# Performance work log

Hardware: AMD Instinct MI355X
Metric: run time of the kernel (lower is better)

## Reference

```python
import jax, jax.numpy as jnp
import numpy as np

EMBED_DIM = 1024
NUM_HEADS = 16
D_K = EMBED_DIM // NUM_HEADS
SEQ = 4096
BATCH = 1


def setup_inputs() -> dict:
    key = jax.random.key(0)
    ks = jax.random.split(key, 9)
    s = 1.0 / np.sqrt(EMBED_DIM)
    return {
        "x": jax.random.normal(ks[0], (BATCH, SEQ, EMBED_DIM), dtype=jnp.float32),
        "Wq": jax.random.normal(ks[1], (EMBED_DIM, EMBED_DIM), dtype=jnp.float32) * s,
        "bq": jax.random.normal(ks[2], (EMBED_DIM,), dtype=jnp.float32) * 0.02,
        "Wk": jax.random.normal(ks[3], (EMBED_DIM, EMBED_DIM), dtype=jnp.float32) * s,
        "bk": jax.random.normal(ks[4], (EMBED_DIM,), dtype=jnp.float32) * 0.02,
        "Wv": jax.random.normal(ks[5], (EMBED_DIM, EMBED_DIM), dtype=jnp.float32) * s,
        "bv": jax.random.normal(ks[6], (EMBED_DIM,), dtype=jnp.float32) * 0.02,
        "Wo": jax.random.normal(ks[7], (EMBED_DIM, EMBED_DIM), dtype=jnp.float32) * s,
        "bo": jax.random.normal(ks[8], (EMBED_DIM,), dtype=jnp.float32) * 0.02,
    }


def reference(x, Wq, bq, Wk, bk, Wv, bv, Wo, bo):
    B, S, E = x.shape
    H, Dk = NUM_HEADS, D_K

    def split_heads(t):  # [B,S,E] -> [B,H,S,Dk]
        return t.reshape(B, S, H, Dk).transpose(0, 2, 1, 3)

    Q = split_heads(x @ Wq.T + bq)
    K = split_heads(x @ Wk.T + bk)
    V = split_heads(x @ Wv.T + bv)

    scores = jnp.einsum("bhqd,bhkd->bhqk", Q, K) / jnp.sqrt(jnp.float32(Dk))
    causal = jnp.tril(jnp.ones((S, S), dtype=bool))
    scores = jnp.where(causal, scores, -jnp.inf)
    attn = jax.nn.softmax(scores, axis=-1)
    out = jnp.einsum("bhqk,bhkd->bhqd", attn, V)  # [B,H,S,Dk]
    out = out.transpose(0, 2, 1, 3).reshape(B, S, E)
    return out @ Wo.T + bo
```

## Files before the change

### kernel.cpp

```cpp
#include <hip/hip_runtime.h>
#include <hip/hip_bf16.h>
#include <math.h>

#define SEQ 4096
#define EMB 1024
#define NH  16
#define DK  64

typedef __attribute__((ext_vector_type(8))) unsigned short us8;
typedef __attribute__((ext_vector_type(8))) short         s8;
typedef __attribute__((ext_vector_type(4))) unsigned short us4;
typedef __attribute__((ext_vector_type(4))) float          f4;

static __device__ __forceinline__ unsigned short f2bf(float f) {
    union { float f; unsigned u; } v; v.f = f;
    unsigned r = v.u + 0x7FFF + ((v.u >> 16) & 1);
    return (unsigned short)(r >> 16);
}

__device__ __forceinline__ void gl2lds16(const void* g, void* l) {
    __builtin_amdgcn_global_load_lds((const __attribute__((address_space(1))) void*)g,
                                     (__attribute__((address_space(3))) void*)l, 16, 0, 0);
}

__device__ __forceinline__ int pkbf(float a, float b) {
    return (int)__builtin_amdgcn_perm(__float_as_uint(a), __float_as_uint(b), 0x07060302u);
}

__global__ void cvt_all(const float* __restrict__ x,
                        const float* __restrict__ w0, const float* __restrict__ w1,
                        const float* __restrict__ w2, const float* __restrict__ w3,
                        unsigned short* __restrict__ xo,
                        unsigned short* __restrict__ o0, unsigned short* __restrict__ o1,
                        unsigned short* __restrict__ o2, unsigned short* __restrict__ o3) {
    const int idx = blockIdx.x * 256 + threadIdx.x;
    const float* in;
    unsigned short* out;
    int off;
    if (idx < (1 << 20)) { in = x; out = xo; off = idx; }
    else {
        const int t = idx - (1 << 20);
        const int w = t >> 18;
        off = t & ((1 << 18) - 1);
        in  = w == 0 ? w0 : (w == 1 ? w1 : (w == 2 ? w2 : w3));
        out = w == 0 ? o0 : (w == 1 ? o1 : (w == 2 ? o2 : o3));
    }
    const float4 v = ((const float4*)in)[off];
    us4 o;
    o[0] = f2bf(v.x); o[1] = f2bf(v.y); o[2] = f2bf(v.z); o[3] = f2bf(v.w);
    ((us4*)out)[off] = o;
}

__global__ __launch_bounds__(256) void transpose_kernel(
    const unsigned short* __restrict__ in, unsigned short* __restrict__ out) {
    __shared__ unsigned short t[64][72];
    const int tid = threadIdx.x;
    const int row = tid >> 2, c = (tid & 3) * 16;
    const int gr = blockIdx.x * 64, gc = blockIdx.y * 64;
    const unsigned short* src = in + (size_t)(gr + row) * EMB + gc + c;
    *(us8*)&t[row][c]     = *(const us8*)src;
    *(us8*)&t[row][c + 8] = *(const us8*)(src + 8);
    __syncthreads();
    us8 o0, o1;
#pragma unroll
    for (int j = 0; j < 8; ++j) { o0[j] = t[c + j][row]; o1[j] = t[c + 8 + j][row]; }
    unsigned short* dst = out + (size_t)(gc + row) * SEQ + gr + c;
    *(us8*)dst       = o0;
    *(us8*)(dst + 8) = o1;
}

__global__ __launch_bounds__(256) void qkv_gemm(
    const unsigned short* __restrict__ X,
    const unsigned short* __restrict__ Wq, const unsigned short* __restrict__ Wk,
    const unsigned short* __restrict__ Wv,
    const float* __restrict__ bq, const float* __restrict__ bk, const float* __restrict__ bv,
    unsigned short* __restrict__ Qo, unsigned short* __restrict__ Ko, unsigned short* __restrict__ Vo)
{
    __shared__ unsigned short As[128 * 64];
    __shared__ unsigned short Bs[128 * 64];

    const int region = blockIdx.y >> 3;
    const unsigned short* W   = region == 0 ? Wq : (region == 1 ? Wk : Wv);
    const float*         bias = region == 0 ? bq : (region == 1 ? bk : bv);
    unsigned short*      out  = region == 0 ? Qo : (region == 1 ? Ko : Vo);
    const float scale = region == 0 ? 0.18033688011112042f : 1.0f;

    const int tid  = threadIdx.x;
    const int wave = tid >> 6;
    const int lane = tid & 63;
    const int quad = lane >> 4;
    const int l16  = lane & 15;
    const int wm   = (wave >> 1) * 64;
    const int wn   = (wave & 1) * 64;
    const int bm   = blockIdx.x * 128;
    const int bn   = (blockIdx.y & 7) * 128;

    f4 acc[4][4];
#pragma unroll
    for (int a = 0; a < 4; ++a)
#pragma unroll
        for (int b = 0; b < 4; ++b) acc[a][b] = (f4){0, 0, 0, 0};

    const int rsub = lane >> 3;
    const int gc   = ((lane & 7) ^ rsub) * 8;
    const int swz  = l16 & 7;

    for (int k0 = 0; k0 < EMB; k0 += 64) {
        __syncthreads();
#pragma unroll
        for (int i = 0; i < 4; ++i) {
            const int cb = i * 4 + wave;
            const int r  = cb * 8 + rsub;
            gl2lds16(X + (size_t)(bm + r) * EMB + k0 + gc, &As[cb * 512]);
            gl2lds16(W + (size_t)(bn + r) * EMB + k0 + gc, &Bs[cb * 512]);
        }
        __syncthreads();
#pragma unroll
        for (int kc = 0; kc < 2; ++kc) {
            s8 af[4], bf[4];
#pragma unroll
            for (int t = 0; t < 4; ++t) {
                const int seg = (kc * 4 + quad) ^ swz;
                af[t] = *(const s8*)&As[(wm + t * 16 + l16) * 64 + seg * 8];
                bf[t] = *(const s8*)&Bs[(wn + t * 16 + l16) * 64 + seg * 8];
            }
#pragma unroll
            for (int tm = 0; tm < 4; ++tm)
#pragma unroll
                for (int tn = 0; tn < 4; ++tn)
                    acc[tm][tn] = __builtin_amdgcn_mfma_f32_16x16x32_bf16(af[tm], bf[tn], acc[tm][tn], 0, 0, 0);
        }
    }

#pragma unroll
    for (int tn = 0; tn < 4; ++tn) {
        const int n = bn + wn + tn * 16 + l16;
        const float bv2 = bias[n];
#pragma unroll
        for (int tm = 0; tm < 4; ++tm)
#pragma unroll
            for (int rr = 0; rr < 4; ++rr) {
                const int m = bm + wm + tm * 16 + quad * 4 + rr;
                out[(size_t)m * EMB + n] = f2bf((acc[tm][tn][rr] + bv2) * scale);
            }
    }
}

__global__ __launch_bounds__(256) void gemm_op(
    const unsigned short* __restrict__ A, const unsigned short* __restrict__ B,
    const float* __restrict__ bias, float* __restrict__ C)
{
    __shared__ unsigned short As[128 * 64];
    __shared__ unsigned short Bs[64 * 64];

    const int tid  = threadIdx.x;
    const int wave = tid >> 6;
    const int lane = tid & 63;
    const int quad = lane >> 4;
    const int l16  = lane & 15;
    const int wm   = (wave >> 1) * 64;
    const int wn   = (wave & 1) * 32;
    const int bm   = blockIdx.x * 128;
    const int bn   = blockIdx.y * 64;

    f4 acc[4][2];
#pragma unroll
    for (int a = 0; a < 4; ++a) { acc[a][0] = (f4){0,0,0,0}; acc[a][1] = (f4){0,0,0,0}; }

    const int rsub = lane >> 3;
    const int gc   = ((lane & 7) ^ rsub) * 8;
    const int swz  = l16 & 7;

    for (int k0 = 0; k0 < EMB; k0 += 64) {
        __syncthreads();
#pragma unroll
        for (int i = 0; i < 6; ++i) {
            const int cb = i * 4 + wave;
            if (cb < 16) {
                gl2lds16(A + (size_t)(bm + cb * 8 + rsub) * EMB + k0 + gc, &As[cb * 512]);
            } else {
                const int c2 = cb - 16;
                gl2lds16(B + (size_t)(bn + c2 * 8 + rsub) * EMB + k0 + gc, &Bs[c2 * 512]);
            }
        }
        __syncthreads();
#pragma unroll
        for (int kc = 0; kc < 2; ++kc) {
            const int seg = (kc * 4 + quad) ^ swz;
            s8 af[4], bf[2];
#pragma unroll
            for (int t = 0; t < 4; ++t)
                af[t] = *(const s8*)&As[(wm + t * 16 + l16) * 64 + seg * 8];
#pragma unroll
            for (int t = 0; t < 2; ++t)
                bf[t] = *(const s8*)&Bs[(wn + t * 16 + l16) * 64 + seg * 8];
#pragma unroll
            for (int tm = 0; tm < 4; ++tm)
#pragma unroll
                for (int tn = 0; tn < 2; ++tn)
                    acc[tm][tn] = __builtin_amdgcn_mfma_f32_16x16x32_bf16(af[tm], bf[tn], acc[tm][tn], 0, 0, 0);
        }
    }

#pragma unroll
    for (int tn = 0; tn < 2; ++tn) {
        const int n = bn + wn + tn * 16 + l16;
        const float bv2 = bias[n];
#pragma unroll
        for (int tm = 0; tm < 4; ++tm)
#pragma unroll
            for (int rr = 0; rr < 4; ++rr) {
                const int m = bm + wm + tm * 16 + quad * 4 + rr;
                C[(size_t)m * EMB + n] = acc[tm][tn][rr] + bv2;
            }
    }
}

__global__ __launch_bounds__(256) void attn_kernel(
    const unsigned short* __restrict__ Qg, const unsigned short* __restrict__ Kg,
    const unsigned short* __restrict__ Vtg, unsigned short* __restrict__ Og)
{
    __shared__ unsigned short Ks[2][64][72];
    __shared__ unsigned short Vs[2][64][72];

    const int tid  = threadIdx.x;
    const int wave = tid >> 6;
    const int lane = tid & 63;
    const int quad = lane >> 4;
    const int l16  = lane & 15;
    const int h    = blockIdx.x;
    const int y    = blockIdx.y;
    const int g    = y >> 4, u = y & 15;
    const int tile = g == 0 ? 63 - u : (g == 1 ? 32 + u : (g == 2 ? 31 - u : u));
    const int colbase = h * DK;
    const int wrow0 = tile * 64 + wave * 16;
    const int q_own = wrow0 + l16;

    s8 qf[2];
    {
        const unsigned short* q = Qg + (size_t)q_own * EMB + colbase + quad * 8;
        qf[0] = *(const s8*)(q);
        qf[1] = *(const s8*)(q + 32);
    }

    const int row = tid >> 2;
    const int c0  = (tid & 3) * 16;
    const int a_    = c0 >> 4;
    const int vcol0 = (a_ >> 1) * 32 + (a_ & 1) * 4;

    const unsigned short* kptr = Kg  + (size_t)row * EMB + colbase + c0;
    const unsigned short* vptr = Vtg + (size_t)(colbase + row) * SEQ + c0;

    const int jmax = tile;
    us8 kr0 = *(const us8*)kptr, kr1 = *(const us8*)(kptr + 8);
    us8 vr0 = *(const us8*)vptr, vr1 = *(const us8*)(vptr + 8);
    {
        *(us8*)&Ks[0][row][c0]     = kr0;
        *(us8*)&Ks[0][row][c0 + 8] = kr1;
        us4 w0, w1, w2, w3;
#pragma unroll
        for (int i = 0; i < 4; ++i) { w0[i] = vr0[i]; w1[i] = vr0[4+i]; w2[i] = vr1[i]; w3[i] = vr1[4+i]; }
        *(us4*)&Vs[0][row][vcol0]      = w0;
        *(us4*)&Vs[0][row][vcol0 + 8]  = w1;
        *(us4*)&Vs[0][row][vcol0 + 16] = w2;
        *(us4*)&Vs[0][row][vcol0 + 24] = w3;
    }
    kr0 = *(const us8*)(kptr + (size_t)64 * EMB);
    kr1 = *(const us8*)(kptr + (size_t)64 * EMB + 8);
    vr0 = *(const us8*)(vptr + 64);
    vr1 = *(const us8*)(vptr + 64 + 8);

    float l_i = 0.0f;
    f4 o[4];
#pragma unroll
    for (int t = 0; t < 4; ++t) o[t] = (f4){0, 0, 0, 0};

    for (int j = 0; j <= jmax; ++j) {
        __syncthreads();
        const int cur = j & 1;
        if (j < jmax) {
            const int nxt = cur ^ 1;
            *(us8*)&Ks[nxt][row][c0]     = kr0;
            *(us8*)&Ks[nxt][row][c0 + 8] = kr1;
            us4 w0, w1, w2, w3;
#pragma unroll
            for (int i = 0; i < 4; ++i) { w0[i] = vr0[i]; w1[i] = vr0[4+i]; w2[i] = vr1[i]; w3[i] = vr1[4+i]; }
            *(us4*)&Vs[nxt][row][vcol0]      = w0;
            *(us4*)&Vs[nxt][row][vcol0 + 8]  = w1;
            *(us4*)&Vs[nxt][row][vcol0 + 16] = w2;
            *(us4*)&Vs[nxt][row][vcol0 + 24] = w3;
            if (j + 1 < jmax) {
                const unsigned short* kn = kptr + (size_t)(j + 2) * 64 * EMB;
                const unsigned short* vn = vptr + (j + 2) * 64;
                kr0 = *(const us8*)kn;  kr1 = *(const us8*)(kn + 8);
                vr0 = *(const us8*)vn;  vr1 = *(const us8*)(vn + 8);
            }
        }

        f4 s[4] = { {0,0,0,0}, {0,0,0,0}, {0,0,0,0}, {0,0,0,0} };
#pragma unroll
        for (int kc = 0; kc < 2; ++kc)
#pragma unroll
            for (int t = 0; t < 4; ++t) {
                s8 kv = *(const s8*)&Ks[cur][t * 16 + l16][kc * 32 + quad * 8];
                s[t] = __builtin_amdgcn_mfma_f32_16x16x32_bf16(kv, qf[kc], s[t], 0, 0, 0);
            }

        if (j == jmax) {
#pragma unroll
            for (int t = 0; t < 4; ++t) {
                const int kb = j * 64 + t * 16 + quad * 4;
#pragma unroll
                for (int r = 0; r < 4; ++r)
                    if (kb + r > q_own) s[t][r] = -1e30f;
            }
        }

        float rs = 0.0f;
#pragma unroll
        for (int t = 0; t < 4; ++t)
#pragma unroll
            for (int r = 0; r < 4; ++r) {
                const float p = __builtin_amdgcn_exp2f(s[t][r]);
                s[t][r] = p;
                rs += p;
            }
        rs += __shfl_xor(rs, 16);
        rs += __shfl_xor(rs, 32);
        l_i += rs;

        union { int i[8]; s8 v[2]; } pku;
#pragma unroll
        for (int t = 0; t < 4; ++t) {
            pku.i[t * 2]     = pkbf(s[t][1], s[t][0]);
            pku.i[t * 2 + 1] = pkbf(s[t][3], s[t][2]);
        }

#pragma unroll
        for (int kc = 0; kc < 2; ++kc)
#pragma unroll
            for (int t = 0; t < 4; ++t) {
                s8 va = *(const s8*)&Vs[cur][t * 16 + l16][kc * 32 + quad * 8];
                o[t] = __builtin_amdgcn_mfma_f32_16x16x32_bf16(va, pku.v[kc], o[t], 0, 0, 0);
            }
    }

    const float inv = 1.0f / l_i;
#pragma unroll
    for (int t = 0; t < 4; ++t) {
        us4 ov;
#pragma unroll
        for (int r = 0; r < 4; ++r) ov[r] = f2bf(o[t][r] * inv);
        *(us4*)&Og[(size_t)q_own * EMB + colbase + t * 16 + quad * 4] = ov;
    }
}

extern "C" void kernel_launch(void* const* d_in, const int* in_sizes, int n_in,
                              void* d_out, int out_size, void* d_ws, size_t ws_size,
                              hipStream_t stream) {
    const float* x  = (const float*)d_in[0];
    const float* Wq = (const float*)d_in[1];
    const float* bq = (const float*)d_in[2];
    const float* Wk = (const float*)d_in[3];
    const float* bk = (const float*)d_in[4];
    const float* Wv = (const float*)d_in[5];
    const float* bv = (const float*)d_in[6];
    const float* Wo = (const float*)d_in[7];
    const float* bo = (const float*)d_in[8];
    float* out = (float*)d_out;

    unsigned short* ws = (unsigned short*)d_ws;
    unsigned short* xb  = ws;
    unsigned short* Wqb = xb  + (size_t)SEQ * EMB;
    unsigned short* Wkb = Wqb + (size_t)EMB * EMB;
    unsigned short* Wvb = Wkb + (size_t)EMB * EMB;
    unsigned short* Wob = Wvb + (size_t)EMB * EMB;
    unsigned short* Qb  = Wob + (size_t)EMB * EMB;
    unsigned short* Kb  = Qb  + (size_t)SEQ * EMB;
    unsigned short* Vtb = Kb  + (size_t)SEQ * EMB;
    unsigned short* Ab  = Vtb + (size_t)SEQ * EMB;

    cvt_all<<<8192, 256, 0, stream>>>(x, Wq, Wk, Wv, Wo, xb, Wqb, Wkb, Wvb, Wob);

    qkv_gemm<<<dim3(SEQ / 128, 24), 256, 0, stream>>>(xb, Wqb, Wkb, Wvb, bq, bk, bv, Qb, Kb, Ab);

    transpose_kernel<<<dim3(SEQ / 64, EMB / 64), 256, 0, stream>>>(Ab, Vtb);

    attn_kernel<<<dim3(NH, 64), 256, 0, stream>>>(Qb, Kb, Vtb, Ab);

    gemm_op<<<dim3(SEQ / 128, EMB / 64), 256, 0, stream>>>(Ab, Wob, bo, out);
}
```

Measured before the change: 216.3 us.

## Pair complementary causal query tiles per attention block and move V column permute into transpose

Each attention block now runs 512 threads covering two query tiles (u and 63-u), so every block does an equal amount of causal work and shares the same K/V tile loads between both tiles. Waves for the shorter tile skip compute once their diagonal is reached but still help load shared tiles. The V column permutation used by the MFMA layout moves from the attention kernel's LDS store into the transpose kernel's global store, which simplifies the per-iteration staging to one 16-byte store each for K and V. The trade-off is larger blocks with idle waves in later iterations and fewer blocks in the grid.

```diff
diff --git a/kernel.cpp b/kernel.cpp
--- a/kernel.cpp
+++ b/kernel.cpp
@@ -64,9 +64,16 @@
     us8 o0, o1;
 #pragma unroll
     for (int j = 0; j < 8; ++j) { o0[j] = t[c + j][row]; o1[j] = t[c + 8 + j][row]; }
-    unsigned short* dst = out + (size_t)(gc + row) * SEQ + gr + c;
-    *(us8*)dst       = o0;
-    *(us8*)(dst + 8) = o1;
+    const int a_   = c >> 4;
+    const int base = (a_ >> 1) * 32 + (a_ & 1) * 4;
+    us4 g0, g1, g2, g3;
+#pragma unroll
+    for (int i = 0; i < 4; ++i) { g0[i] = o0[i]; g1[i] = o0[4 + i]; g2[i] = o1[i]; g3[i] = o1[4 + i]; }
+    unsigned short* dst = out + (size_t)(gc + row) * SEQ + gr + base;
+    *(us4*)dst        = g0;
+    *(us4*)(dst + 8)  = g1;
+    *(us4*)(dst + 16) = g2;
+    *(us4*)(dst + 24) = g3;
 }
 
 __global__ __launch_bounds__(256) void qkv_gemm(
@@ -216,7 +223,7 @@
     }
 }
 
-__global__ __launch_bounds__(256) void attn_kernel(
+__global__ __launch_bounds__(512) void attn_kernel(
     const unsigned short* __restrict__ Qg, const unsigned short* __restrict__ Kg,
     const unsigned short* __restrict__ Vtg, unsigned short* __restrict__ Og)
 {
@@ -230,10 +237,12 @@
     const int l16  = lane & 15;
     const int h    = blockIdx.x;
     const int y    = blockIdx.y;
-    const int g    = y >> 4, u = y & 15;
-    const int tile = g == 0 ? 63 - u : (g == 1 ? 32 + u : (g == 2 ? 31 - u : u));
+    const int u    = (y < 16) ? y : 47 - y;
+    const int jmax = 63 - u;
+    const int tileMine = (wave < 4) ? (63 - u) : u;
+    const int jmine    = (wave < 4) ? jmax : u;
     const int colbase = h * DK;
-    const int wrow0 = tile * 64 + wave * 16;
+    const int wrow0 = tileMine * 64 + (wave & 3) * 16;
     const int q_own = wrow0 + l16;
 
     s8 qf[2];
@@ -243,32 +252,17 @@
         qf[1] = *(const s8*)(q + 32);
     }
 
-    const int row = tid >> 2;
-    const int c0  = (tid & 3) * 16;
-    const int a_    = c0 >> 4;
-    const int vcol0 = (a_ >> 1) * 32 + (a_ & 1) * 4;
-
+    const int row = tid >> 3;
+    const int c0  = (tid & 7) * 8;
     const unsigned short* kptr = Kg  + (size_t)row * EMB + colbase + c0;
     const unsigned short* vptr = Vtg + (size_t)(colbase + row) * SEQ + c0;
 
-    const int jmax = tile;
-    us8 kr0 = *(const us8*)kptr, kr1 = *(const us8*)(kptr + 8);
-    us8 vr0 = *(const us8*)vptr, vr1 = *(const us8*)(vptr + 8);
-    {
-        *(us8*)&Ks[0][row][c0]     = kr0;
-        *(us8*)&Ks[0][row][c0 + 8] = kr1;
-        us4 w0, w1, w2, w3;
-#pragma unroll
-        for (int i = 0; i < 4; ++i) { w0[i] = vr0[i]; w1[i] = vr0[4+i]; w2[i] = vr1[i]; w3[i] = vr1[4+i]; }
-        *(us4*)&Vs[0][row][vcol0]      = w0;
-        *(us4*)&Vs[0][row][vcol0 + 8]  = w1;
-        *(us4*)&Vs[0][row][vcol0 + 16] = w2;
-        *(us4*)&Vs[0][row][vcol0 + 24] = w3;
-    }
-    kr0 = *(const us8*)(kptr + (size_t)64 * EMB);
-    kr1 = *(const us8*)(kptr + (size_t)64 * EMB + 8);
-    vr0 = *(const us8*)(vptr + 64);
-    vr1 = *(const us8*)(vptr + 64 + 8);
+    us8 kr = *(const us8*)kptr;
+    us8 vr = *(const us8*)vptr;
+    *(us8*)&Ks[0][row][c0] = kr;
+    *(us8*)&Vs[0][row][c0] = vr;
+    kr = *(const us8*)(kptr + (size_t)64 * EMB);
+    vr = *(const us8*)(vptr + 64);
 
     float l_i = 0.0f;
     f4 o[4];
@@ -280,69 +274,62 @@
         const int cur = j & 1;
         if (j < jmax) {
             const int nxt = cur ^ 1;
-            *(us8*)&Ks[nxt][row][c0]     = kr0;
-            *(us8*)&Ks[nxt][row][c0 + 8] = kr1;
-            us4 w0, w1, w2, w3;
-#pragma unroll
-            for (int i = 0; i < 4; ++i) { w0[i] = vr0[i]; w1[i] = vr0[4+i]; w2[i] = vr1[i]; w3[i] = vr1[4+i]; }
-            *(us4*)&Vs[nxt][row][vcol0]      = w0;
-            *(us4*)&Vs[nxt][row][vcol0 + 8]  = w1;
-            *(us4*)&Vs[nxt][row][vcol0 + 16] = w2;
-            *(us4*)&Vs[nxt][row][vcol0 + 24] = w3;
+            *(us8*)&Ks[nxt][row][c0] = kr;
+            *(us8*)&Vs[nxt][row][c0] = vr;
             if (j + 1 < jmax) {
-                const unsigned short* kn = kptr + (size_t)(j + 2) * 64 * EMB;
-                const unsigned short* vn = vptr + (j + 2) * 64;
-                kr0 = *(const us8*)kn;  kr1 = *(const us8*)(kn + 8);
-                vr0 = *(const us8*)vn;  vr1 = *(const us8*)(vn + 8);
-            }
-        }
-
-        f4 s[4] = { {0,0,0,0}, {0,0,0,0}, {0,0,0,0}, {0,0,0,0} };
-#pragma unroll
-        for (int kc = 0; kc < 2; ++kc)
+                kr = *(const us8*)(kptr + (size_t)(j + 2) * 64 * EMB);
+                vr = *(const us8*)(vptr + (j + 2) * 64);
+            }
+        }
+
+        if (j <= jmine) {
+            f4 s[4] = { {0,0,0,0}, {0,0,0,0}, {0,0,0,0}, {0,0,0,0} };
+#pragma unroll
+            for (int kc = 0; kc < 2; ++kc)
+#pragma unroll
+                for (int t = 0; t < 4; ++t) {
+                    s8 kv = *(const s8*)&Ks[cur][t * 16 + l16][kc * 32 + quad * 8];
+                    s[t] = __builtin_amdgcn_mfma_f32_16x16x32_bf16(kv, qf[kc], s[t], 0, 0, 0);
+                }
+
+            if (j == jmine) {
+#pragma unroll
+                for (int t = 0; t < 4; ++t) {
+                    const int kb = j * 64 + t * 16 + quad * 4;
+#pragma unroll
+                    for (int r = 0; r < 4; ++r)
+                        if (kb + r > q_own) s[t][r] = -1e30f;
+                }
+            }
+
+            float rs = 0.0f;
+#pragma unroll
+            for (int t = 0; t < 4; ++t)
+#pragma unroll
+                for (int r = 0; r < 4; ++r) {
+                    const float p = __builtin_amdgcn_exp2f(s[t][r]);
+                    s[t][r] = p;
+                    rs += p;
+                }
+            rs += __shfl_xor(rs, 16);
+            rs += __shfl_xor(rs, 32);
+            l_i += rs;
+
+            union { int i[8]; s8 v[2]; } pku;
 #pragma unroll
             for (int t = 0; t < 4; ++t) {
-                s8 kv = *(const s8*)&Ks[cur][t * 16 + l16][kc * 32 + quad * 8];
-                s[t] = __builtin_amdgcn_mfma_f32_16x16x32_bf16(kv, qf[kc], s[t], 0, 0, 0);
-            }
-
-        if (j == jmax) {
-#pragma unroll
-            for (int t = 0; t < 4; ++t) {
-                const int kb = j * 64 + t * 16 + quad * 4;
-#pragma unroll
-                for (int r = 0; r < 4; ++r)
-                    if (kb + r > q_own) s[t][r] = -1e30f;
-            }
-        }
-
-        float rs = 0.0f;
-#pragma unroll
-        for (int t = 0; t < 4; ++t)
-#pragma unroll
-            for (int r = 0; r < 4; ++r) {
-                const float p = __builtin_amdgcn_exp2f(s[t][r]);
-                s[t][r] = p;
-                rs += p;
-            }
-        rs += __shfl_xor(rs, 16);
-        rs += __shfl_xor(rs, 32);
-        l_i += rs;
-
-        union { int i[8]; s8 v[2]; } pku;
-#pragma unroll
-        for (int t = 0; t < 4; ++t) {
-            pku.i[t * 2]     = pkbf(s[t][1], s[t][0]);
-            pku.i[t * 2 + 1] = pkbf(s[t][3], s[t][2]);
-        }
-
-#pragma unroll
-        for (int kc = 0; kc < 2; ++kc)
-#pragma unroll
-            for (int t = 0; t < 4; ++t) {
-                s8 va = *(const s8*)&Vs[cur][t * 16 + l16][kc * 32 + quad * 8];
-                o[t] = __builtin_amdgcn_mfma_f32_16x16x32_bf16(va, pku.v[kc], o[t], 0, 0, 0);
-            }
+                pku.i[t * 2]     = pkbf(s[t][1], s[t][0]);
+                pku.i[t * 2 + 1] = pkbf(s[t][3], s[t][2]);
+            }
+
+#pragma unroll
+            for (int kc = 0; kc < 2; ++kc)
+#pragma unroll
+                for (int t = 0; t < 4; ++t) {
+                    s8 va = *(const s8*)&Vs[cur][t * 16 + l16][kc * 32 + quad * 8];
+                    o[t] = __builtin_amdgcn_mfma_f32_16x16x32_bf16(va, pku.v[kc], o[t], 0, 0, 0);
+                }
+        }
     }
 
     const float inv = 1.0f / l_i;
@@ -386,7 +373,7 @@
 
     transpose_kernel<<<dim3(SEQ / 64, EMB / 64), 256, 0, stream>>>(Ab, Vtb);
 
-    attn_kernel<<<dim3(NH, 64), 256, 0, stream>>>(Qb, Kb, Vtb, Ab);
+    attn_kernel<<<dim3(NH, 32), 512, 0, stream>>>(Qb, Kb, Vtb, Ab);
 
     gemm_op<<<dim3(SEQ / 128, EMB / 64), 256, 0, stream>>>(Ab, Wob, bo, out);
 }
```

Result: faster. 209.6 us (-3.1%).
